# Kernel optimization log

Measured on AMD Instinct MI355X. Metric: run time of the kernel, lower is better.

Reference implementation:

```python
import jax, jax.numpy as jnp
import numpy as np

T = 5          # Newton iterations (init kwarg T)
EPS = 1e-05    # covariance regularizer (init kwarg eps)


def setup_inputs() -> dict:
    key = jax.random.key(0)
    k1, k2 = jax.random.split(key)
    B, C, H, W = 64, 128, 56, 56
    x = jax.random.normal(k1, (B, C, H, W), dtype=jnp.float32)
    running_rot = jax.random.normal(k2, (C, C), dtype=jnp.float32)
    return {"x": x, "running_rot": running_rot}


def reference(x, running_rot):
    # Concept Whitening forward (training-mode batch statistics), channels_first.
    # 1) IterNorm ZCA whitening via T Newton iterations on the CxC covariance.
    # 2) Rotation by the (non-trainable) running rotation matrix.
    B, C, H, W = x.shape
    m = B * H * W
    # (C, m): channels as rows, all samples/locations as columns
    xt = x.transpose(1, 0, 2, 3).reshape(C, m)
    mean = jnp.mean(xt, axis=1, keepdims=True)
    xc = xt - mean
    I = jnp.eye(C, dtype=x.dtype)
    Sigma = EPS * I + (xc @ xc.T) / m            # (C, C)
    rTr = 1.0 / jnp.trace(Sigma)                 # trace normalization
    SigmaN = Sigma * rTr
    P = I
    for _ in range(T):                           # Newton iteration for Sigma^{-1/2}
        P = 0.5 * (3.0 * P - P @ P @ P @ SigmaN)
    wm = P * jnp.sqrt(rTr)                       # whitening matrix Sigma^{-1/2}
    xn = wm @ xc                                 # whitened activations (C, m)
    x_hat = xn.reshape(C, B, H, W).transpose(1, 0, 2, 3)  # (B, C, H, W)
    # rotate into concept-aligned basis: out[b,d,h,w] = sum_c rot[d,c] * x_hat[b,c,h,w]
    out = jnp.einsum('bchw,dc->bdhw', x_hat, running_rot)
    return out
```

## Files before the change

### kernel.cpp

```cpp
#include <hip/hip_runtime.h>
#include <math.h>

#define HW 3136
#define NCHUNK 3136
#define M_TOT 200704.0f
#define EPSV 1e-5f

typedef __attribute__((ext_vector_type(8))) short bf16x8;
typedef __attribute__((ext_vector_type(4))) short short4v;
typedef __attribute__((ext_vector_type(4))) float f32x4;

__device__ inline unsigned short f2bf(float f) {
  unsigned u = __float_as_uint(f);
  u += 0x7FFFu + ((u >> 16) & 1u);
  return (unsigned short)(u >> 16);
}

__global__ __launch_bounds__(512, 4) void gram_k(const float* __restrict__ x,
                                                 float* __restrict__ partG,
                                                 float* __restrict__ S,
                                                 int slots) {
  __shared__ unsigned short xs[2][128 * 72];
  const int t = threadIdx.x;
  const int lm = t & 15, quad = (t >> 4) & 3, w = t >> 6;
  const int row0 = w * 16;
  const int qofs = (t & 15) * 4;
  const int chi = t >> 4;

  f32x4 acc[8];
  f32x4 sacc;
  const f32x4 z = {0.f, 0.f, 0.f, 0.f};
  sacc = z;
#pragma unroll
  for (int j = 0; j < 8; ++j) acc[j] = z;
  bf16x8 ones;
#pragma unroll
  for (int j = 0; j < 8; ++j) ones[j] = (short)0x3F80;

  int chunk = blockIdx.x;
  float4 pre[4];
  {
    const int b = chunk / 49;
    const int s0 = (chunk % 49) * 64;
    const float* base = x + (size_t)(b * 128) * HW + s0;
#pragma unroll
    for (int i = 0; i < 4; ++i)
      pre[i] = *(const float4*)(base + (size_t)(i * 32 + chi) * HW + qofs);
  }

  int buf = 0;
  while (chunk < NCHUNK) {
#pragma unroll
    for (int i = 0; i < 4; ++i) {
      const int c = i * 32 + chi;
      uint2 dw;
      dw.x = (unsigned)f2bf(pre[i].x) | ((unsigned)f2bf(pre[i].y) << 16);
      dw.y = (unsigned)f2bf(pre[i].z) | ((unsigned)f2bf(pre[i].w) << 16);
      *(uint2*)&xs[buf][c * 72 + qofs] = dw;
    }
    __syncthreads();
    const int nxt = chunk + slots;
    if (nxt < NCHUNK) {
      const int b = nxt / 49;
      const int s0 = (nxt % 49) * 64;
      const float* base = x + (size_t)(b * 128) * HW + s0;
#pragma unroll
      for (int i = 0; i < 4; ++i)
        pre[i] = *(const float4*)(base + (size_t)(i * 32 + chi) * HW + qofs);
    }
#pragma unroll
    for (int ks = 0; ks < 2; ++ks) {
      const int ko = ks * 32 + quad * 8;
      const bf16x8 a0 = *(const bf16x8*)&xs[buf][(row0 + lm) * 72 + ko];
      sacc = __builtin_amdgcn_mfma_f32_16x16x32_bf16(a0, ones, sacc, 0, 0, 0);
#pragma unroll
      for (int tj = 0; tj < 8; ++tj) {
        const bf16x8 bf = *(const bf16x8*)&xs[buf][(tj * 16 + lm) * 72 + ko];
        acc[tj] = __builtin_amdgcn_mfma_f32_16x16x32_bf16(a0, bf, acc[tj], 0, 0, 0);
      }
    }
    buf ^= 1;
    chunk = nxt;
  }

  float* pg = partG + (size_t)blockIdx.x * 16384;
#pragma unroll
  for (int tj = 0; tj < 8; ++tj)
#pragma unroll
    for (int r = 0; r < 4; ++r)
      pg[(row0 + quad * 4 + r) * 128 + tj * 16 + lm] = acc[tj][r];
  if (lm == 0) {
#pragma unroll
    for (int r = 0; r < 4; ++r)
      atomicAdd(&S[row0 + quad * 4 + r], sacc[r]);
  }
}

__global__ __launch_bounds__(256) void gsig_k(const float* __restrict__ partG,
                                              const float* __restrict__ S,
                                              float* __restrict__ Sigma,
                                              float* __restrict__ trace,
                                              int slots) {
  __shared__ float4 red[256];
  const int t = threadIdx.x;
  const int q = t & 31;
  const int h = t >> 5;
  const int b = blockIdx.x;
  const float* base = partG + (size_t)b * 128 + 4 * q;
  float ax = 0.f, ay = 0.f, az = 0.f, aw = 0.f;
#pragma unroll 8
  for (int s = h; s < slots; s += 8) {
    const float4 v = *(const float4*)(base + (size_t)s * 16384);
    ax += v.x; ay += v.y; az += v.z; aw += v.w;
  }
  red[t] = make_float4(ax, ay, az, aw);
  __syncthreads();
  if (t < 128) {
    const float4 o = red[t + 128];
    red[t].x += o.x; red[t].y += o.y; red[t].z += o.z; red[t].w += o.w;
  }
  __syncthreads();
  if (t < 64) {
    const float4 o = red[t + 64];
    red[t].x += o.x; red[t].y += o.y; red[t].z += o.z; red[t].w += o.w;
  }
  __syncthreads();
  if (t < 32) {
    const float4 g0 = red[t];
    const float4 g1 = red[t + 32];
    const float rm = 1.0f / M_TOT;
    const float sb = S[b] * rm;
    const float4 s4 = *(const float4*)(S + 4 * t);
    float o[4];
    o[0] = (g0.x + g1.x - sb * s4.x) * rm;
    o[1] = (g0.y + g1.y - sb * s4.y) * rm;
    o[2] = (g0.z + g1.z - sb * s4.z) * rm;
    o[3] = (g0.w + g1.w - sb * s4.w) * rm;
    if (t == (b >> 2)) {
      o[b & 3] += EPSV;
      atomicAdd(trace, o[b & 3]);
    }
    *(float4*)(Sigma + b * 128 + 4 * t) = make_float4(o[0], o[1], o[2], o[3]);
  }
}

__global__ __launch_bounds__(512) void newton1_k(const float* __restrict__ Sig,
                                                 const float* __restrict__ trace,
                                                 float* __restrict__ Pout) {
  __shared__ float s1[8 * 132];
  __shared__ float s2[8 * 132];
  __shared__ float red[512 * 17];
  const int t = threadIdx.x;
  const int ct = t & 31;
  const int rt = (t >> 5) & 1;
  const int kt = t >> 6;
  const int k0 = kt * 16;
  const int rg0 = blockIdx.x * 8;
  const int ra = rg0 + 4 * rt;
  const float rTr = 1.0f / *trace;
  const float nh = -0.5f * rTr;
  float a[4][4];

#pragma unroll
  for (int i = 0; i < 4; ++i)
#pragma unroll
    for (int j = 0; j < 4; ++j) a[i][j] = 0.f;
#pragma unroll 4
  for (int k = k0; k < k0 + 16; ++k) {
    const float4 sa4 = *(const float4*)(Sig + k * 128 + ra);
    const float4 sb4 = *(const float4*)(Sig + k * 128 + 4 * ct);
    float aA[4] = {nh * sa4.x, nh * sa4.y, nh * sa4.z, nh * sa4.w};
    float bA[4] = {nh * sb4.x, nh * sb4.y, nh * sb4.z, nh * sb4.w};
#pragma unroll
    for (int i = 0; i < 4; ++i) if (ra + i == k) aA[i] += 1.5f;
#pragma unroll
    for (int j = 0; j < 4; ++j) if (4 * ct + j == k) bA[j] += 1.5f;
#pragma unroll
    for (int i = 0; i < 4; ++i)
#pragma unroll
      for (int j = 0; j < 4; ++j) a[i][j] += aA[i] * bA[j];
  }
#pragma unroll
  for (int i = 0; i < 4; ++i)
#pragma unroll
    for (int j = 0; j < 4; ++j) red[t * 17 + i * 4 + j] = a[i][j];
  __syncthreads();
  if (t < 64) {
#pragma unroll
    for (int u = 1; u < 8; ++u)
#pragma unroll
      for (int i = 0; i < 4; ++i)
#pragma unroll
        for (int j = 0; j < 4; ++j)
          a[i][j] += red[(t + 64 * u) * 17 + i * 4 + j];
#pragma unroll
    for (int i = 0; i < 4; ++i)
#pragma unroll
      for (int j = 0; j < 4; ++j)
        s1[(4 * rt + i) * 132 + 4 * ct + j] = a[i][j];
  }
  __syncthreads();

#pragma unroll
  for (int i = 0; i < 4; ++i)
#pragma unroll
    for (int j = 0; j < 4; ++j) a[i][j] = 0.f;
#pragma unroll 4
  for (int k = k0; k < k0 + 16; ++k) {
    float aA[4];
#pragma unroll
    for (int i = 0; i < 4; ++i) aA[i] = s1[(4 * rt + i) * 132 + k];
    const float4 sb4 = *(const float4*)(Sig + k * 128 + 4 * ct);
    float bA[4] = {nh * sb4.x, nh * sb4.y, nh * sb4.z, nh * sb4.w};
#pragma unroll
    for (int j = 0; j < 4; ++j) if (4 * ct + j == k) bA[j] += 1.5f;
#pragma unroll
    for (int i = 0; i < 4; ++i)
#pragma unroll
      for (int j = 0; j < 4; ++j) a[i][j] += aA[i] * bA[j];
  }
  __syncthreads();
#pragma unroll
  for (int i = 0; i < 4; ++i)
#pragma unroll
    for (int j = 0; j < 4; ++j) red[t * 17 + i * 4 + j] = a[i][j];
  __syncthreads();
  if (t < 64) {
#pragma unroll
    for (int u = 1; u < 8; ++u)
#pragma unroll
      for (int i = 0; i < 4; ++i)
#pragma unroll
        for (int j = 0; j < 4; ++j)
          a[i][j] += red[(t + 64 * u) * 17 + i * 4 + j];
#pragma unroll
    for (int i = 0; i < 4; ++i)
#pragma unroll
      for (int j = 0; j < 4; ++j)
        s2[(4 * rt + i) * 132 + 4 * ct + j] = a[i][j];
  }
  __syncthreads();

#pragma unroll
  for (int i = 0; i < 4; ++i)
#pragma unroll
    for (int j = 0; j < 4; ++j) a[i][j] = 0.f;
#pragma unroll 4
  for (int k = k0; k < k0 + 16; ++k) {
    float aA[4];
#pragma unroll
    for (int i = 0; i < 4; ++i) aA[i] = s2[(4 * rt + i) * 132 + k];
    const float4 bv = *(const float4*)(Sig + k * 128 + 4 * ct);
    const float bA[4] = {bv.x, bv.y, bv.z, bv.w};
#pragma unroll
    for (int i = 0; i < 4; ++i)
#pragma unroll
      for (int j = 0; j < 4; ++j) a[i][j] += aA[i] * bA[j];
  }
  __syncthreads();
#pragma unroll
  for (int i = 0; i < 4; ++i)
#pragma unroll
    for (int j = 0; j < 4; ++j) red[t * 17 + i * 4 + j] = a[i][j];
  __syncthreads();
  if (t < 64) {
#pragma unroll
    for (int u = 1; u < 8; ++u)
#pragma unroll
      for (int i = 0; i < 4; ++i)
#pragma unroll
        for (int j = 0; j < 4; ++j)
          a[i][j] += red[(t + 64 * u) * 17 + i * 4 + j];
#pragma unroll
    for (int i = 0; i < 4; ++i) {
      const int rg = rg0 + 4 * rt + i;
      const float4 sv = *(const float4*)(Sig + rg * 128 + 4 * ct);
      float p1v[4] = {nh * sv.x, nh * sv.y, nh * sv.z, nh * sv.w};
#pragma unroll
      for (int j = 0; j < 4; ++j) if (4 * ct + j == rg) p1v[j] += 1.5f;
      *(float4*)(Pout + rg * 128 + 4 * ct) =
          make_float4(0.5f * (3.f * p1v[0] - rTr * a[i][0]),
                      0.5f * (3.f * p1v[1] - rTr * a[i][1]),
                      0.5f * (3.f * p1v[2] - rTr * a[i][2]),
                      0.5f * (3.f * p1v[3] - rTr * a[i][3]));
    }
  }
}

__global__ __launch_bounds__(512) void newton_k(const float* __restrict__ P,
                                                const float* __restrict__ Sig,
                                                const float* __restrict__ trace,
                                                float* __restrict__ Pout) {
  __shared__ float s1[8 * 132];
  __shared__ float s2[8 * 132];
  __shared__ float red[512 * 17];
  const int t = threadIdx.x;
  const int ct = t & 31;
  const int rt = (t >> 5) & 1;
  const int kt = t >> 6;
  const int k0 = kt * 16;
  const int rg0 = blockIdx.x * 8;
  const float rTr = 1.0f / *trace;
  float a[4][4];

#pragma unroll
  for (int i = 0; i < 4; ++i)
#pragma unroll
    for (int j = 0; j < 4; ++j) a[i][j] = 0.f;
#pragma unroll 4
  for (int k = k0; k < k0 + 16; ++k) {
    const float4 av = *(const float4*)(P + k * 128 + rg0 + 4 * rt);
    const float4 bv = *(const float4*)(P + k * 128 + 4 * ct);
    const float aA[4] = {av.x, av.y, av.z, av.w};
    const float bA[4] = {bv.x, bv.y, bv.z, bv.w};
#pragma unroll
    for (int i = 0; i < 4; ++i)
#pragma unroll
      for (int j = 0; j < 4; ++j) a[i][j] += aA[i] * bA[j];
  }
#pragma unroll
  for (int i = 0; i < 4; ++i)
#pragma unroll
    for (int j = 0; j < 4; ++j) red[t * 17 + i * 4 + j] = a[i][j];
  __syncthreads();
  if (t < 64) {
#pragma unroll
    for (int u = 1; u < 8; ++u)
#pragma unroll
      for (int i = 0; i < 4; ++i)
#pragma unroll
        for (int j = 0; j < 4; ++j)
          a[i][j] += red[(t + 64 * u) * 17 + i * 4 + j];
#pragma unroll
    for (int i = 0; i < 4; ++i)
#pragma unroll
      for (int j = 0; j < 4; ++j)
        s1[(4 * rt + i) * 132 + 4 * ct + j] = a[i][j];
  }
  __syncthreads();

#pragma unroll
  for (int i = 0; i < 4; ++i)
#pragma unroll
    for (int j = 0; j < 4; ++j) a[i][j] = 0.f;
#pragma unroll 4
  for (int k = k0; k < k0 + 16; ++k) {
    float aA[4];
#pragma unroll
    for (int i = 0; i < 4; ++i) aA[i] = s1[(4 * rt + i) * 132 + k];
    const float4 bv = *(const float4*)(P + k * 128 + 4 * ct);
    const float bA[4] = {bv.x, bv.y, bv.z, bv.w};
#pragma unroll
    for (int i = 0; i < 4; ++i)
#pragma unroll
      for (int j = 0; j < 4; ++j) a[i][j] += aA[i] * bA[j];
  }
  __syncthreads();
#pragma unroll
  for (int i = 0; i < 4; ++i)
#pragma unroll
    for (int j = 0; j < 4; ++j) red[t * 17 + i * 4 + j] = a[i][j];
  __syncthreads();
  if (t < 64) {
#pragma unroll
    for (int u = 1; u < 8; ++u)
#pragma unroll
      for (int i = 0; i < 4; ++i)
#pragma unroll
        for (int j = 0; j < 4; ++j)
          a[i][j] += red[(t + 64 * u) * 17 + i * 4 + j];
#pragma unroll
    for (int i = 0; i < 4; ++i)
#pragma unroll
      for (int j = 0; j < 4; ++j)
        s2[(4 * rt + i) * 132 + 4 * ct + j] = a[i][j];
  }
  __syncthreads();

#pragma unroll
  for (int i = 0; i < 4; ++i)
#pragma unroll
    for (int j = 0; j < 4; ++j) a[i][j] = 0.f;
#pragma unroll 4
  for (int k = k0; k < k0 + 16; ++k) {
    float aA[4];
#pragma unroll
    for (int i = 0; i < 4; ++i) aA[i] = s2[(4 * rt + i) * 132 + k];
    const float4 bv = *(const float4*)(Sig + k * 128 + 4 * ct);
    const float bA[4] = {bv.x, bv.y, bv.z, bv.w};
#pragma unroll
    for (int i = 0; i < 4; ++i)
#pragma unroll
      for (int j = 0; j < 4; ++j) a[i][j] += aA[i] * bA[j];
  }
  __syncthreads();
#pragma unroll
  for (int i = 0; i < 4; ++i)
#pragma unroll
    for (int j = 0; j < 4; ++j) red[t * 17 + i * 4 + j] = a[i][j];
  __syncthreads();
  if (t < 64) {
#pragma unroll
    for (int u = 1; u < 8; ++u)
#pragma unroll
      for (int i = 0; i < 4; ++i)
#pragma unroll
        for (int j = 0; j < 4; ++j)
          a[i][j] += red[(t + 64 * u) * 17 + i * 4 + j];
#pragma unroll
    for (int i = 0; i < 4; ++i) {
      const int rg = rg0 + 4 * rt + i;
      const float4 pv = *(const float4*)(P + rg * 128 + 4 * ct);
      *(float4*)(Pout + rg * 128 + 4 * ct) =
          make_float4(0.5f * (3.f * pv.x - rTr * a[i][0]),
                      0.5f * (3.f * pv.y - rTr * a[i][1]),
                      0.5f * (3.f * pv.z - rTr * a[i][2]),
                      0.5f * (3.f * pv.w - rTr * a[i][3]));
    }
  }
}

__global__ __launch_bounds__(256) void rotmt_k(const float* __restrict__ rot,
                                               const float* __restrict__ P,
                                               const float* __restrict__ S,
                                               const float* __restrict__ trace,
                                               unsigned short* __restrict__ Mbf,
                                               float* __restrict__ bias) {
  const int t = threadIdx.x;
  const int r = t >> 5;
  const int dg = blockIdx.x * 8 + r;
  const int c0 = (t & 31) * 4;
  const float* rrow = rot + dg * 128;
  const float sc = sqrtf(1.0f / *trace);

  float ax = 0, ay = 0, az = 0, aw = 0;
#pragma unroll 4
  for (int k = 0; k < 128; ++k) {
    const float a = rrow[k];
    const float4 bv = *(const float4*)(P + k * 128 + c0);
    ax += a * bv.x; ay += a * bv.y; az += a * bv.z; aw += a * bv.w;
  }
  ax *= sc; ay *= sc; az *= sc; aw *= sc;
  uint2 dw;
  dw.x = (unsigned)f2bf(ax) | ((unsigned)f2bf(ay) << 16);
  dw.y = (unsigned)f2bf(az) | ((unsigned)f2bf(aw) << 16);
  *(uint2*)&Mbf[dg * 128 + c0] = dw;
  const float4 sv = *(const float4*)(S + c0);
  float p = (ax * sv.x + ay * sv.y + az * sv.z + aw * sv.w) * (1.0f / M_TOT);
  for (int off = 16; off > 0; off >>= 1) p += __shfl_down(p, off, 32);
  if ((t & 31) == 0) bias[dg] = p;
}

#define MSTR 136
#define XSTR 132
__global__ __launch_bounds__(256, 3) void apply_k(const float* __restrict__ x,
                                                  const unsigned short* __restrict__ Mbf,
                                                  const float* __restrict__ bias,
                                                  float* __restrict__ out) {
  __shared__ unsigned short Ms[128 * MSTR];
  __shared__ unsigned short xsB[64 * XSTR];
  const int t = threadIdx.x;
  const int lm = t & 15, quad = (t >> 4) & 3, w = t >> 6;
  const int b = blockIdx.x / 49;
  const int s0 = (blockIdx.x % 49) * 64;

#pragma unroll
  for (int i = 0; i < 8; ++i) {
    const int e = i * 256 + t;
    const int row = e >> 4, oct = e & 15;
    *(uint4*)&Ms[row * MSTR + oct * 8] =
        *(const uint4*)(Mbf + row * 128 + oct * 8);
  }
#pragma unroll
  for (int i = 0; i < 4; ++i) {
    const int p = 16 * i + (t >> 4);
    const int q = t & 15;
    const float* px = x + (size_t)(b * 128 + 2 * p) * HW + s0 + 4 * q;
    const float4 fa = *(const float4*)px;
    const float4 fb = *(const float4*)(px + HW);
    const float faA[4] = {fa.x, fa.y, fa.z, fa.w};
    const float fbA[4] = {fb.x, fb.y, fb.z, fb.w};
#pragma unroll
    for (int r = 0; r < 4; ++r) {
      const unsigned dw =
          (unsigned)f2bf(faA[r]) | ((unsigned)f2bf(fbA[r]) << 16);
      *(unsigned*)&xsB[(4 * q + r) * XSTR + 2 * p] = dw;
    }
  }
  float biasr[2][4];
#pragma unroll
  for (int i = 0; i < 2; ++i)
#pragma unroll
    for (int r = 0; r < 4; ++r)
      biasr[i][r] = bias[(2 * w + i) * 16 + quad * 4 + r];
  __syncthreads();

  const f32x4 z = {0.f, 0.f, 0.f, 0.f};
  f32x4 acc[2][4];
#pragma unroll
  for (int i = 0; i < 2; ++i)
#pragma unroll
    for (int sj = 0; sj < 4; ++sj) acc[i][sj] = z;

#pragma unroll
  for (int ks = 0; ks < 4; ++ks) {
    const int ko = ks * 32 + quad * 8;
    const bf16x8 a0 = *(const bf16x8*)&Ms[((2 * w + 0) * 16 + lm) * MSTR + ko];
    const bf16x8 a1 = *(const bf16x8*)&Ms[((2 * w + 1) * 16 + lm) * MSTR + ko];
#pragma unroll
    for (int sj = 0; sj < 4; ++sj) {
      const short4v blo = *(const short4v*)&xsB[(sj * 16 + lm) * XSTR + ko];
      const short4v bhi = *(const short4v*)&xsB[(sj * 16 + lm) * XSTR + ko + 4];
      const bf16x8 bf = __builtin_shufflevector(blo, bhi, 0, 1, 2, 3, 4, 5, 6, 7);
      acc[0][sj] = __builtin_amdgcn_mfma_f32_16x16x32_bf16(a0, bf, acc[0][sj], 0, 0, 0);
      acc[1][sj] = __builtin_amdgcn_mfma_f32_16x16x32_bf16(a1, bf, acc[1][sj], 0, 0, 0);
    }
  }
#pragma unroll
  for (int i = 0; i < 2; ++i)
#pragma unroll
    for (int r = 0; r < 4; ++r) {
      const int d = (2 * w + i) * 16 + quad * 4 + r;
      float* orow = out + (size_t)(b * 128 + d) * HW + s0 + lm;
#pragma unroll
      for (int sj = 0; sj < 4; ++sj)
        orow[sj * 16] = acc[i][sj][r] - biasr[i][r];
    }
}

extern "C" void kernel_launch(void* const* d_in, const int* in_sizes, int n_in,
                              void* d_out, int out_size, void* d_ws,
                              size_t ws_size, hipStream_t stream) {
  const float* x = (const float*)d_in[0];
  const float* rot = (const float*)d_in[1];
  float* out = (float*)d_out;
  float* ws = (float*)d_ws;

  float* Sigma  = ws;
  float* Pa     = ws + 16384;
  float* Pb     = ws + 32768;
  unsigned short* Mbf = (unsigned short*)(ws + 49152);
  float* S      = ws + 57344;
  float* trace  = ws + 57472;
  float* bias   = ws + 57488;
  float* partG  = ws + 57616;

  const size_t wsf = ws_size / 4;
  long avail = (long)wsf - 57616;
  int slots = (int)(avail / 16384);
  if (slots > 512) slots = 512;
  if (slots < 1) slots = 1;

  hipMemsetAsync(S, 0, 129 * 4, stream);

  gram_k<<<slots, 512, 0, stream>>>(x, partG, S, slots);
  gsig_k<<<128, 256, 0, stream>>>(partG, S, Sigma, trace, slots);
  newton1_k<<<16, 512, 0, stream>>>(Sigma, trace, Pb);
  newton_k<<<16, 512, 0, stream>>>(Pb, Sigma, trace, Pa);
  newton_k<<<16, 512, 0, stream>>>(Pa, Sigma, trace, Pb);
  newton_k<<<16, 512, 0, stream>>>(Pb, Sigma, trace, Pa);
  rotmt_k<<<16, 256, 0, stream>>>(rot, Pa, S, trace, Mbf, bias);
  apply_k<<<3136, 256, 0, stream>>>(x, Mbf, bias, out);
}
```

Before: 299.6 us.

## Fuse covariance reduction, Newton iterations and rotation into one persistent kernel

Replaces the chain of small kernels (gsig, four Newton kernels, rotmt) with a single 128-block kernel that uses software grid barriers built from atomic counters. Per-block row sums are written to a partial buffer and reduced in the kernel instead of atomically added to S. The intent is to remove the launch gaps between the tiny serial stages. The cost is spin-wait barriers that rely on all 128 blocks being co-resident. Newton work now runs on only 16 blocks of 256 threads, each thread covering a longer k range.

```diff
diff --git a/kernel.cpp b/kernel.cpp
--- a/kernel.cpp
+++ b/kernel.cpp
@@ -18,7 +18,7 @@
 
 __global__ __launch_bounds__(512, 4) void gram_k(const float* __restrict__ x,
                                                  float* __restrict__ partG,
-                                                 float* __restrict__ S,
+                                                 float* __restrict__ partS,
                                                  int slots) {
   __shared__ unsigned short xs[2][128 * 72];
   const int t = threadIdx.x;
@@ -92,73 +92,30 @@
   if (lm == 0) {
 #pragma unroll
     for (int r = 0; r < 4; ++r)
-      atomicAdd(&S[row0 + quad * 4 + r], sacc[r]);
-  }
-}
-
-__global__ __launch_bounds__(256) void gsig_k(const float* __restrict__ partG,
-                                              const float* __restrict__ S,
-                                              float* __restrict__ Sigma,
-                                              float* __restrict__ trace,
-                                              int slots) {
-  __shared__ float4 red[256];
-  const int t = threadIdx.x;
-  const int q = t & 31;
-  const int h = t >> 5;
-  const int b = blockIdx.x;
-  const float* base = partG + (size_t)b * 128 + 4 * q;
-  float ax = 0.f, ay = 0.f, az = 0.f, aw = 0.f;
-#pragma unroll 8
-  for (int s = h; s < slots; s += 8) {
-    const float4 v = *(const float4*)(base + (size_t)s * 16384);
-    ax += v.x; ay += v.y; az += v.z; aw += v.w;
-  }
-  red[t] = make_float4(ax, ay, az, aw);
-  __syncthreads();
-  if (t < 128) {
-    const float4 o = red[t + 128];
-    red[t].x += o.x; red[t].y += o.y; red[t].z += o.z; red[t].w += o.w;
-  }
-  __syncthreads();
-  if (t < 64) {
-    const float4 o = red[t + 64];
-    red[t].x += o.x; red[t].y += o.y; red[t].z += o.z; red[t].w += o.w;
-  }
-  __syncthreads();
-  if (t < 32) {
-    const float4 g0 = red[t];
-    const float4 g1 = red[t + 32];
-    const float rm = 1.0f / M_TOT;
-    const float sb = S[b] * rm;
-    const float4 s4 = *(const float4*)(S + 4 * t);
-    float o[4];
-    o[0] = (g0.x + g1.x - sb * s4.x) * rm;
-    o[1] = (g0.y + g1.y - sb * s4.y) * rm;
-    o[2] = (g0.z + g1.z - sb * s4.z) * rm;
-    o[3] = (g0.w + g1.w - sb * s4.w) * rm;
-    if (t == (b >> 2)) {
-      o[b & 3] += EPSV;
-      atomicAdd(trace, o[b & 3]);
-    }
-    *(float4*)(Sigma + b * 128 + 4 * t) = make_float4(o[0], o[1], o[2], o[3]);
-  }
-}
-
-__global__ __launch_bounds__(512) void newton1_k(const float* __restrict__ Sig,
-                                                 const float* __restrict__ trace,
-                                                 float* __restrict__ Pout) {
-  __shared__ float s1[8 * 132];
-  __shared__ float s2[8 * 132];
-  __shared__ float red[512 * 17];
-  const int t = threadIdx.x;
+      partS[blockIdx.x * 128 + row0 + quad * 4 + r] = sacc[r];
+  }
+}
+
+__device__ inline void gbar(unsigned* c, unsigned n) {
+  __syncthreads();
+  __threadfence();
+  if (threadIdx.x == 0) {
+    __hip_atomic_fetch_add(c, 1u, __ATOMIC_RELEASE, __HIP_MEMORY_SCOPE_AGENT);
+    while (__hip_atomic_load(c, __ATOMIC_ACQUIRE, __HIP_MEMORY_SCOPE_AGENT) < n)
+      __builtin_amdgcn_s_sleep(8);
+  }
+  __syncthreads();
+  __threadfence();
+}
+
+__device__ inline void newton_step(const float* __restrict__ P,
+                                   const float* __restrict__ Sig,
+                                   float rTr, float* __restrict__ Pout,
+                                   int rg0, int t, float* s1, float* s2,
+                                   float* red) {
   const int ct = t & 31;
   const int rt = (t >> 5) & 1;
   const int kt = t >> 6;
-  const int k0 = kt * 16;
-  const int rg0 = blockIdx.x * 8;
-  const int ra = rg0 + 4 * rt;
-  const float rTr = 1.0f / *trace;
-  const float nh = -0.5f * rTr;
   float a[4][4];
 
 #pragma unroll
@@ -166,149 +123,7 @@
 #pragma unroll
     for (int j = 0; j < 4; ++j) a[i][j] = 0.f;
 #pragma unroll 4
-  for (int k = k0; k < k0 + 16; ++k) {
-    const float4 sa4 = *(const float4*)(Sig + k * 128 + ra);
-    const float4 sb4 = *(const float4*)(Sig + k * 128 + 4 * ct);
-    float aA[4] = {nh * sa4.x, nh * sa4.y, nh * sa4.z, nh * sa4.w};
-    float bA[4] = {nh * sb4.x, nh * sb4.y, nh * sb4.z, nh * sb4.w};
-#pragma unroll
-    for (int i = 0; i < 4; ++i) if (ra + i == k) aA[i] += 1.5f;
-#pragma unroll
-    for (int j = 0; j < 4; ++j) if (4 * ct + j == k) bA[j] += 1.5f;
-#pragma unroll
-    for (int i = 0; i < 4; ++i)
-#pragma unroll
-      for (int j = 0; j < 4; ++j) a[i][j] += aA[i] * bA[j];
-  }
-#pragma unroll
-  for (int i = 0; i < 4; ++i)
-#pragma unroll
-    for (int j = 0; j < 4; ++j) red[t * 17 + i * 4 + j] = a[i][j];
-  __syncthreads();
-  if (t < 64) {
-#pragma unroll
-    for (int u = 1; u < 8; ++u)
-#pragma unroll
-      for (int i = 0; i < 4; ++i)
-#pragma unroll
-        for (int j = 0; j < 4; ++j)
-          a[i][j] += red[(t + 64 * u) * 17 + i * 4 + j];
-#pragma unroll
-    for (int i = 0; i < 4; ++i)
-#pragma unroll
-      for (int j = 0; j < 4; ++j)
-        s1[(4 * rt + i) * 132 + 4 * ct + j] = a[i][j];
-  }
-  __syncthreads();
-
-#pragma unroll
-  for (int i = 0; i < 4; ++i)
-#pragma unroll
-    for (int j = 0; j < 4; ++j) a[i][j] = 0.f;
-#pragma unroll 4
-  for (int k = k0; k < k0 + 16; ++k) {
-    float aA[4];
-#pragma unroll
-    for (int i = 0; i < 4; ++i) aA[i] = s1[(4 * rt + i) * 132 + k];
-    const float4 sb4 = *(const float4*)(Sig + k * 128 + 4 * ct);
-    float bA[4] = {nh * sb4.x, nh * sb4.y, nh * sb4.z, nh * sb4.w};
-#pragma unroll
-    for (int j = 0; j < 4; ++j) if (4 * ct + j == k) bA[j] += 1.5f;
-#pragma unroll
-    for (int i = 0; i < 4; ++i)
-#pragma unroll
-      for (int j = 0; j < 4; ++j) a[i][j] += aA[i] * bA[j];
-  }
-  __syncthreads();
-#pragma unroll
-  for (int i = 0; i < 4; ++i)
-#pragma unroll
-    for (int j = 0; j < 4; ++j) red[t * 17 + i * 4 + j] = a[i][j];
-  __syncthreads();
-  if (t < 64) {
-#pragma unroll
-    for (int u = 1; u < 8; ++u)
-#pragma unroll
-      for (int i = 0; i < 4; ++i)
-#pragma unroll
-        for (int j = 0; j < 4; ++j)
-          a[i][j] += red[(t + 64 * u) * 17 + i * 4 + j];
-#pragma unroll
-    for (int i = 0; i < 4; ++i)
-#pragma unroll
-      for (int j = 0; j < 4; ++j)
-        s2[(4 * rt + i) * 132 + 4 * ct + j] = a[i][j];
-  }
-  __syncthreads();
-
-#pragma unroll
-  for (int i = 0; i < 4; ++i)
-#pragma unroll
-    for (int j = 0; j < 4; ++j) a[i][j] = 0.f;
-#pragma unroll 4
-  for (int k = k0; k < k0 + 16; ++k) {
-    float aA[4];
-#pragma unroll
-    for (int i = 0; i < 4; ++i) aA[i] = s2[(4 * rt + i) * 132 + k];
-    const float4 bv = *(const float4*)(Sig + k * 128 + 4 * ct);
-    const float bA[4] = {bv.x, bv.y, bv.z, bv.w};
-#pragma unroll
-    for (int i = 0; i < 4; ++i)
-#pragma unroll
-      for (int j = 0; j < 4; ++j) a[i][j] += aA[i] * bA[j];
-  }
-  __syncthreads();
-#pragma unroll
-  for (int i = 0; i < 4; ++i)
-#pragma unroll
-    for (int j = 0; j < 4; ++j) red[t * 17 + i * 4 + j] = a[i][j];
-  __syncthreads();
-  if (t < 64) {
-#pragma unroll
-    for (int u = 1; u < 8; ++u)
-#pragma unroll
-      for (int i = 0; i < 4; ++i)
-#pragma unroll
-        for (int j = 0; j < 4; ++j)
-          a[i][j] += red[(t + 64 * u) * 17 + i * 4 + j];
-#pragma unroll
-    for (int i = 0; i < 4; ++i) {
-      const int rg = rg0 + 4 * rt + i;
-      const float4 sv = *(const float4*)(Sig + rg * 128 + 4 * ct);
-      float p1v[4] = {nh * sv.x, nh * sv.y, nh * sv.z, nh * sv.w};
-#pragma unroll
-      for (int j = 0; j < 4; ++j) if (4 * ct + j == rg) p1v[j] += 1.5f;
-      *(float4*)(Pout + rg * 128 + 4 * ct) =
-          make_float4(0.5f * (3.f * p1v[0] - rTr * a[i][0]),
-                      0.5f * (3.f * p1v[1] - rTr * a[i][1]),
-                      0.5f * (3.f * p1v[2] - rTr * a[i][2]),
-                      0.5f * (3.f * p1v[3] - rTr * a[i][3]));
-    }
-  }
-}
-
-__global__ __launch_bounds__(512) void newton_k(const float* __restrict__ P,
-                                                const float* __restrict__ Sig,
-                                                const float* __restrict__ trace,
-                                                float* __restrict__ Pout) {
-  __shared__ float s1[8 * 132];
-  __shared__ float s2[8 * 132];
-  __shared__ float red[512 * 17];
-  const int t = threadIdx.x;
-  const int ct = t & 31;
-  const int rt = (t >> 5) & 1;
-  const int kt = t >> 6;
-  const int k0 = kt * 16;
-  const int rg0 = blockIdx.x * 8;
-  const float rTr = 1.0f / *trace;
-  float a[4][4];
-
-#pragma unroll
-  for (int i = 0; i < 4; ++i)
-#pragma unroll
-    for (int j = 0; j < 4; ++j) a[i][j] = 0.f;
-#pragma unroll 4
-  for (int k = k0; k < k0 + 16; ++k) {
+  for (int k = kt * 32; k < kt * 32 + 32; ++k) {
     const float4 av = *(const float4*)(P + k * 128 + rg0 + 4 * rt);
     const float4 bv = *(const float4*)(P + k * 128 + 4 * ct);
     const float aA[4] = {av.x, av.y, av.z, av.w};
@@ -325,7 +140,7 @@
   __syncthreads();
   if (t < 64) {
 #pragma unroll
-    for (int u = 1; u < 8; ++u)
+    for (int u = 1; u < 4; ++u)
 #pragma unroll
       for (int i = 0; i < 4; ++i)
 #pragma unroll
@@ -344,7 +159,7 @@
 #pragma unroll
     for (int j = 0; j < 4; ++j) a[i][j] = 0.f;
 #pragma unroll 4
-  for (int k = k0; k < k0 + 16; ++k) {
+  for (int k = kt * 32; k < kt * 32 + 32; ++k) {
     float aA[4];
 #pragma unroll
     for (int i = 0; i < 4; ++i) aA[i] = s1[(4 * rt + i) * 132 + k];
@@ -363,7 +178,7 @@
   __syncthreads();
   if (t < 64) {
 #pragma unroll
-    for (int u = 1; u < 8; ++u)
+    for (int u = 1; u < 4; ++u)
 #pragma unroll
       for (int i = 0; i < 4; ++i)
 #pragma unroll
@@ -382,7 +197,7 @@
 #pragma unroll
     for (int j = 0; j < 4; ++j) a[i][j] = 0.f;
 #pragma unroll 4
-  for (int k = k0; k < k0 + 16; ++k) {
+  for (int k = kt * 32; k < kt * 32 + 32; ++k) {
     float aA[4];
 #pragma unroll
     for (int i = 0; i < 4; ++i) aA[i] = s2[(4 * rt + i) * 132 + k];
@@ -401,7 +216,7 @@
   __syncthreads();
   if (t < 64) {
 #pragma unroll
-    for (int u = 1; u < 8; ++u)
+    for (int u = 1; u < 4; ++u)
 #pragma unroll
       for (int i = 0; i < 4; ++i)
 #pragma unroll
@@ -420,35 +235,247 @@
   }
 }
 
-__global__ __launch_bounds__(256) void rotmt_k(const float* __restrict__ rot,
-                                               const float* __restrict__ P,
-                                               const float* __restrict__ S,
-                                               const float* __restrict__ trace,
-                                               unsigned short* __restrict__ Mbf,
-                                               float* __restrict__ bias) {
+__device__ inline void newton1_step(const float* __restrict__ Sig, float rTr,
+                                    float* __restrict__ Pout, int rg0, int t,
+                                    float* s1, float* s2, float* red) {
+  const int ct = t & 31;
+  const int rt = (t >> 5) & 1;
+  const int kt = t >> 6;
+  const int ra = rg0 + 4 * rt;
+  const float nh = -0.5f * rTr;
+  float a[4][4];
+
+#pragma unroll
+  for (int i = 0; i < 4; ++i)
+#pragma unroll
+    for (int j = 0; j < 4; ++j) a[i][j] = 0.f;
+#pragma unroll 4
+  for (int k = kt * 32; k < kt * 32 + 32; ++k) {
+    const float4 sa4 = *(const float4*)(Sig + k * 128 + ra);
+    const float4 sb4 = *(const float4*)(Sig + k * 128 + 4 * ct);
+    float aA[4] = {nh * sa4.x, nh * sa4.y, nh * sa4.z, nh * sa4.w};
+    float bA[4] = {nh * sb4.x, nh * sb4.y, nh * sb4.z, nh * sb4.w};
+#pragma unroll
+    for (int i = 0; i < 4; ++i) if (ra + i == k) aA[i] += 1.5f;
+#pragma unroll
+    for (int j = 0; j < 4; ++j) if (4 * ct + j == k) bA[j] += 1.5f;
+#pragma unroll
+    for (int i = 0; i < 4; ++i)
+#pragma unroll
+      for (int j = 0; j < 4; ++j) a[i][j] += aA[i] * bA[j];
+  }
+#pragma unroll
+  for (int i = 0; i < 4; ++i)
+#pragma unroll
+    for (int j = 0; j < 4; ++j) red[t * 17 + i * 4 + j] = a[i][j];
+  __syncthreads();
+  if (t < 64) {
+#pragma unroll
+    for (int u = 1; u < 4; ++u)
+#pragma unroll
+      for (int i = 0; i < 4; ++i)
+#pragma unroll
+        for (int j = 0; j < 4; ++j)
+          a[i][j] += red[(t + 64 * u) * 17 + i * 4 + j];
+#pragma unroll
+    for (int i = 0; i < 4; ++i)
+#pragma unroll
+      for (int j = 0; j < 4; ++j)
+        s1[(4 * rt + i) * 132 + 4 * ct + j] = a[i][j];
+  }
+  __syncthreads();
+
+#pragma unroll
+  for (int i = 0; i < 4; ++i)
+#pragma unroll
+    for (int j = 0; j < 4; ++j) a[i][j] = 0.f;
+#pragma unroll 4
+  for (int k = kt * 32; k < kt * 32 + 32; ++k) {
+    float aA[4];
+#pragma unroll
+    for (int i = 0; i < 4; ++i) aA[i] = s1[(4 * rt + i) * 132 + k];
+    const float4 sb4 = *(const float4*)(Sig + k * 128 + 4 * ct);
+    float bA[4] = {nh * sb4.x, nh * sb4.y, nh * sb4.z, nh * sb4.w};
+#pragma unroll
+    for (int j = 0; j < 4; ++j) if (4 * ct + j == k) bA[j] += 1.5f;
+#pragma unroll
+    for (int i = 0; i < 4; ++i)
+#pragma unroll
+      for (int j = 0; j < 4; ++j) a[i][j] += aA[i] * bA[j];
+  }
+  __syncthreads();
+#pragma unroll
+  for (int i = 0; i < 4; ++i)
+#pragma unroll
+    for (int j = 0; j < 4; ++j) red[t * 17 + i * 4 + j] = a[i][j];
+  __syncthreads();
+  if (t < 64) {
+#pragma unroll
+    for (int u = 1; u < 4; ++u)
+#pragma unroll
+      for (int i = 0; i < 4; ++i)
+#pragma unroll
+        for (int j = 0; j < 4; ++j)
+          a[i][j] += red[(t + 64 * u) * 17 + i * 4 + j];
+#pragma unroll
+    for (int i = 0; i < 4; ++i)
+#pragma unroll
+      for (int j = 0; j < 4; ++j)
+        s2[(4 * rt + i) * 132 + 4 * ct + j] = a[i][j];
+  }
+  __syncthreads();
+
+#pragma unroll
+  for (int i = 0; i < 4; ++i)
+#pragma unroll
+    for (int j = 0; j < 4; ++j) a[i][j] = 0.f;
+#pragma unroll 4
+  for (int k = kt * 32; k < kt * 32 + 32; ++k) {
+    float aA[4];
+#pragma unroll
+    for (int i = 0; i < 4; ++i) aA[i] = s2[(4 * rt + i) * 132 + k];
+    const float4 bv = *(const float4*)(Sig + k * 128 + 4 * ct);
+    const float bA[4] = {bv.x, bv.y, bv.z, bv.w};
+#pragma unroll
+    for (int i = 0; i < 4; ++i)
+#pragma unroll
+      for (int j = 0; j < 4; ++j) a[i][j] += aA[i] * bA[j];
+  }
+  __syncthreads();
+#pragma unroll
+  for (int i = 0; i < 4; ++i)
+#pragma unroll
+    for (int j = 0; j < 4; ++j) red[t * 17 + i * 4 + j] = a[i][j];
+  __syncthreads();
+  if (t < 64) {
+#pragma unroll
+    for (int u = 1; u < 4; ++u)
+#pragma unroll
+      for (int i = 0; i < 4; ++i)
+#pragma unroll
+        for (int j = 0; j < 4; ++j)
+          a[i][j] += red[(t + 64 * u) * 17 + i * 4 + j];
+#pragma unroll
+    for (int i = 0; i < 4; ++i) {
+      const int rg = rg0 + 4 * rt + i;
+      const float4 sv = *(const float4*)(Sig + rg * 128 + 4 * ct);
+      float p1v[4] = {nh * sv.x, nh * sv.y, nh * sv.z, nh * sv.w};
+#pragma unroll
+      for (int j = 0; j < 4; ++j) if (4 * ct + j == rg) p1v[j] += 1.5f;
+      *(float4*)(Pout + rg * 128 + 4 * ct) =
+          make_float4(0.5f * (3.f * p1v[0] - rTr * a[i][0]),
+                      0.5f * (3.f * p1v[1] - rTr * a[i][1]),
+                      0.5f * (3.f * p1v[2] - rTr * a[i][2]),
+                      0.5f * (3.f * p1v[3] - rTr * a[i][3]));
+    }
+  }
+}
+
+__global__ __launch_bounds__(256) void mid_k(
+    const float* __restrict__ partG, const float* __restrict__ partS,
+    const float* __restrict__ rot, float* __restrict__ Sigma,
+    float* __restrict__ Pa, float* __restrict__ Pb, float* __restrict__ Pc,
+    float* __restrict__ Pd, float* __restrict__ S, float* __restrict__ trace,
+    unsigned* __restrict__ ctr, unsigned short* __restrict__ Mbf,
+    float* __restrict__ bias, int slots) {
+  __shared__ float s1[8 * 132];
+  __shared__ float s2[8 * 132];
+  __shared__ __align__(16) float red[256 * 17];
   const int t = threadIdx.x;
-  const int r = t >> 5;
-  const int dg = blockIdx.x * 8 + r;
-  const int c0 = (t & 31) * 4;
-  const float* rrow = rot + dg * 128;
-  const float sc = sqrtf(1.0f / *trace);
-
-  float ax = 0, ay = 0, az = 0, aw = 0;
-#pragma unroll 4
-  for (int k = 0; k < 128; ++k) {
-    const float a = rrow[k];
-    const float4 bv = *(const float4*)(P + k * 128 + c0);
-    ax += a * bv.x; ay += a * bv.y; az += a * bv.z; aw += a * bv.w;
-  }
-  ax *= sc; ay *= sc; az *= sc; aw *= sc;
-  uint2 dw;
-  dw.x = (unsigned)f2bf(ax) | ((unsigned)f2bf(ay) << 16);
-  dw.y = (unsigned)f2bf(az) | ((unsigned)f2bf(aw) << 16);
-  *(uint2*)&Mbf[dg * 128 + c0] = dw;
-  const float4 sv = *(const float4*)(S + c0);
-  float p = (ax * sv.x + ay * sv.y + az * sv.z + aw * sv.w) * (1.0f / M_TOT);
-  for (int off = 16; off > 0; off >>= 1) p += __shfl_down(p, off, 32);
-  if ((t & 31) == 0) bias[dg] = p;
+  const int b = blockIdx.x;
+  const unsigned NB = gridDim.x;
+
+  {
+    float sa = 0.f;
+    for (int s = t; s < slots; s += 256) sa += partS[(size_t)s * 128 + b];
+    red[t] = sa;
+    __syncthreads();
+    for (int off = 128; off > 0; off >>= 1) {
+      if (t < off) red[t] += red[t + off];
+      __syncthreads();
+    }
+    if (t == 0) S[b] = red[0];
+  }
+  gbar(&ctr[0], NB);
+
+  {
+    float4* red4 = (float4*)red;
+    const int q = t & 31;
+    const int h = t >> 5;
+    const float* base = partG + (size_t)b * 128 + 4 * q;
+    float ax = 0.f, ay = 0.f, az = 0.f, aw = 0.f;
+#pragma unroll 8
+    for (int s = h; s < slots; s += 8) {
+      const float4 v = *(const float4*)(base + (size_t)s * 16384);
+      ax += v.x; ay += v.y; az += v.z; aw += v.w;
+    }
+    red4[t] = make_float4(ax, ay, az, aw);
+    __syncthreads();
+    if (t < 128) {
+      const float4 o = red4[t + 128];
+      red4[t].x += o.x; red4[t].y += o.y; red4[t].z += o.z; red4[t].w += o.w;
+    }
+    __syncthreads();
+    if (t < 64) {
+      const float4 o = red4[t + 64];
+      red4[t].x += o.x; red4[t].y += o.y; red4[t].z += o.z; red4[t].w += o.w;
+    }
+    __syncthreads();
+    if (t < 32) {
+      const float4 g0 = red4[t];
+      const float4 g1 = red4[t + 32];
+      const float rm = 1.0f / M_TOT;
+      const float sb = S[b] * rm;
+      const float4 s4 = *(const float4*)(S + 4 * t);
+      float o[4];
+      o[0] = (g0.x + g1.x - sb * s4.x) * rm;
+      o[1] = (g0.y + g1.y - sb * s4.y) * rm;
+      o[2] = (g0.z + g1.z - sb * s4.z) * rm;
+      o[3] = (g0.w + g1.w - sb * s4.w) * rm;
+      if (t == (b >> 2)) {
+        o[b & 3] += EPSV;
+        atomicAdd(trace, o[b & 3]);
+      }
+      *(float4*)(Sigma + b * 128 + 4 * t) = make_float4(o[0], o[1], o[2], o[3]);
+    }
+  }
+  gbar(&ctr[1], NB);
+
+  const float rTr = 1.0f / *trace;
+
+  if (b < 16) newton1_step(Sigma, rTr, Pa, b * 8, t, s1, s2, red);
+  gbar(&ctr[2], NB);
+  if (b < 16) newton_step(Pa, Sigma, rTr, Pb, b * 8, t, s1, s2, red);
+  gbar(&ctr[3], NB);
+  if (b < 16) newton_step(Pb, Sigma, rTr, Pc, b * 8, t, s1, s2, red);
+  gbar(&ctr[4], NB);
+  if (b < 16) newton_step(Pc, Sigma, rTr, Pd, b * 8, t, s1, s2, red);
+  gbar(&ctr[5], NB);
+
+  {
+    if (t < 128) s1[t] = rot[b * 128 + t];
+    __syncthreads();
+    const float sc = sqrtf(rTr);
+    const int c = t & 127;
+    const int kh = t >> 7;
+    float a = 0.f;
+#pragma unroll 4
+    for (int k = kh * 64; k < kh * 64 + 64; ++k)
+      a += s1[k] * Pd[(size_t)k * 128 + c];
+    s2[t] = a;
+    __syncthreads();
+    if (t < 128) {
+      const float m = (s2[t] + s2[t + 128]) * sc;
+      Mbf[b * 128 + t] = f2bf(m);
+      s2[t] = m * S[t];
+    }
+    __syncthreads();
+    for (int off = 64; off > 0; off >>= 1) {
+      if (t < off) s2[t] += s2[t + off];
+      __syncthreads();
+    }
+    if (t == 0) bias[b] = s2[0] * (1.0f / M_TOT);
+  }
 }
 
 #define MSTR 136
@@ -539,26 +566,26 @@
   float* Sigma  = ws;
   float* Pa     = ws + 16384;
   float* Pb     = ws + 32768;
-  unsigned short* Mbf = (unsigned short*)(ws + 49152);
-  float* S      = ws + 57344;
-  float* trace  = ws + 57472;
-  float* bias   = ws + 57488;
-  float* partG  = ws + 57616;
+  float* Pc     = ws + 49152;
+  float* Pd     = ws + 65536;
+  unsigned short* Mbf = (unsigned short*)(ws + 81920);
+  float* S      = ws + 90112;
+  float* bias   = ws + 90240;
+  float* trace  = ws + 90368;
+  unsigned* ctr = (unsigned*)(ws + 90369);
+  float* partG  = ws + 90384;
 
   const size_t wsf = ws_size / 4;
-  long avail = (long)wsf - 57616;
-  int slots = (int)(avail / 16384);
+  long avail = (long)wsf - 90384;
+  int slots = (int)(avail / (16384 + 128));
   if (slots > 512) slots = 512;
   if (slots < 1) slots = 1;
-
-  hipMemsetAsync(S, 0, 129 * 4, stream);
-
-  gram_k<<<slots, 512, 0, stream>>>(x, partG, S, slots);
-  gsig_k<<<128, 256, 0, stream>>>(partG, S, Sigma, trace, slots);
-  newton1_k<<<16, 512, 0, stream>>>(Sigma, trace, Pb);
-  newton_k<<<16, 512, 0, stream>>>(Pb, Sigma, trace, Pa);
-  newton_k<<<16, 512, 0, stream>>>(Pa, Sigma, trace, Pb);
-  newton_k<<<16, 512, 0, stream>>>(Pb, Sigma, trace, Pa);
-  rotmt_k<<<16, 256, 0, stream>>>(rot, Pa, S, trace, Mbf, bias);
+  float* partS = partG + (size_t)slots * 16384;
+
+  hipMemsetAsync(trace, 0, 9 * 4, stream);
+
+  gram_k<<<slots, 512, 0, stream>>>(x, partG, partS, slots);
+  mid_k<<<128, 256, 0, stream>>>(partG, partS, rot, Sigma, Pa, Pb, Pc, Pd, S,
+                                 trace, ctr, Mbf, bias, slots);
   apply_k<<<3136, 256, 0, stream>>>(x, Mbf, bias, out);
 }
```

Measured after the change: 409.4 us. 36.7% more time.
